# Kernel optimization log

Measured on AMD Instinct MI355X. Metric: run time of the kernel, lower is better.

Reference implementation:

```python
import jax, jax.numpy as jnp
import numpy as np

DIM = 192
HEADS = 6
WS = (4, 8, 8)  # window size (D, H, W)
N = WS[0] * WS[1] * WS[2]  # 256 tokens per window
NW = 64
B_ = 256  # batch * nW


def _relative_position_index(ws):
    d, h, w = ws
    coords = jnp.stack(jnp.meshgrid(jnp.arange(d), jnp.arange(h), jnp.arange(w), indexing='ij'))
    coords = coords.reshape(3, -1)  # (3, N)
    rel = coords[:, :, None] - coords[:, None, :]  # (3, N, N)
    rel = rel.transpose(1, 2, 0) + jnp.array([d - 1, h - 1, w - 1])
    idx = rel[..., 0] * ((2 * h - 1) * (2 * w - 1)) + rel[..., 1] * (2 * w - 1) + rel[..., 2]
    return idx.astype(jnp.int32)  # (N, N)


def setup_inputs() -> dict:
    key = jax.random.key(0)
    ks = jax.random.split(key, 7)
    table_rows = (2 * WS[0] - 1) * (2 * WS[1] - 1) * (2 * WS[2] - 1)  # 1575
    return {
        'x': jax.random.normal(ks[0], (B_, N, DIM), dtype=jnp.float32),
        'mask': jax.random.normal(ks[1], (NW, N, N), dtype=jnp.float32),
        'qkv_w': jax.random.normal(ks[2], (DIM, 3 * DIM), dtype=jnp.float32) * 0.02,
        'qkv_b': jnp.zeros((3 * DIM,), dtype=jnp.float32),
        'proj_w': jax.random.normal(ks[3], (DIM, DIM), dtype=jnp.float32) * 0.02,
        'proj_b': jnp.zeros((DIM,), dtype=jnp.float32),
        'bias_table': jax.random.normal(ks[4], (table_rows, HEADS), dtype=jnp.float32) * 0.02,
        'rel_index': _relative_position_index(WS),
    }


def reference(x, mask, qkv_w, qkv_b, proj_w, proj_b, bias_table, rel_index):
    B, Ntok, C = x.shape
    hd = C // HEADS
    scale = hd ** (-0.5)
    qkv = (x @ qkv_w + qkv_b).reshape(B, Ntok, 3, HEADS, hd)
    qkv = qkv.transpose(2, 0, 3, 1, 4)  # (3, B, H, N, hd)
    q, k, v = qkv[0], qkv[1], qkv[2]
    attn = jnp.einsum('bhnd,bhmd->bhnm', q * scale, k)  # (B, H, N, N)
    # gathered relative-position bias: (N, N, H) -> (H, N, N)
    bias = bias_table[rel_index.reshape(-1)].reshape(Ntok, Ntok, HEADS).transpose(2, 0, 1)
    attn = attn + bias[None]
    nW = mask.shape[0]
    attn = attn.reshape(B // nW, nW, HEADS, Ntok, Ntok) + mask[None, :, None]
    attn = attn.reshape(B, HEADS, Ntok, Ntok)
    attn = jax.nn.softmax(attn, axis=-1)
    out = jnp.einsum('bhnm,bhmd->bhnd', attn, v)  # (B, H, N, hd)
    out = out.transpose(0, 2, 1, 3).reshape(B, Ntok, C)
    out = out @ proj_w + proj_b
    return out
```

## Files before the change

### kernel.cpp

```cpp
#include <hip/hip_runtime.h>
#include <cstdint>
#include <math.h>

#define DIMC 192
#define NTOK 256
#define HEADS 6
#define HD 32
#define L2E 1.4426950408889634f

typedef __bf16 bf16x8 __attribute__((ext_vector_type(8)));
typedef __bf16 bf16x4 __attribute__((ext_vector_type(4)));
typedef float f32x4 __attribute__((ext_vector_type(4)));

__device__ __forceinline__ void gload_lds16(const __bf16* g, __bf16* l) {
    __builtin_amdgcn_global_load_lds((const __attribute__((address_space(1))) void*)g,
                                     (__attribute__((address_space(3))) void*)l, 16, 0, 0);
}

__global__ void prep(const float* __restrict__ x, __bf16* __restrict__ xb,
                     const float* __restrict__ qkv_w, __bf16* __restrict__ wqt,
                     const float* __restrict__ proj_w, __bf16* __restrict__ wpt,
                     const float* __restrict__ table, const int* __restrict__ rel,
                     __bf16* __restrict__ biasb) {
    const int bid = blockIdx.x, t = threadIdx.x;
    if (bid < 6144) {
        int i = bid * 256 + t;
        float4 a = ((const float4*)x)[i * 2];
        float4 b = ((const float4*)x)[i * 2 + 1];
        bf16x8 o = {(__bf16)a.x, (__bf16)a.y, (__bf16)a.z, (__bf16)a.w,
                    (__bf16)b.x, (__bf16)b.y, (__bf16)b.z, (__bf16)b.w};
        ((bf16x8*)xb)[i] = o;
    } else if (bid < 6576) {
        int i = (bid - 6144) * 256 + t;
        int n = i / DIMC, k = i - n * DIMC;
        wqt[i] = (__bf16)qkv_w[(size_t)k * 576 + n];
    } else if (bid < 6720) {
        int i = (bid - 6576) * 256 + t;
        int n = i / DIMC, k = i - n * DIMC;
        wpt[i] = (__bf16)proj_w[(size_t)k * DIMC + n];
    } else {
        int i = (bid - 6720) * 256 + t;
        int h = i >> 16;
        int r = i & 65535;
        biasb[i] = (__bf16)(table[rel[r] * 6 + h] * L2E);
    }
}

__launch_bounds__(256, 2)
__global__ void qkvbm(const __bf16* __restrict__ A, const __bf16* __restrict__ Wt,
                      const float* __restrict__ bias,
                      __bf16* __restrict__ qo, __bf16* __restrict__ ko, __bf16* __restrict__ vo,
                      const float* __restrict__ mask, const __bf16* __restrict__ biasb,
                      __bf16* __restrict__ bm) {
    __shared__ __bf16 As[256 * 64];
    __shared__ __bf16 Bs[96 * 64];
    const int t = threadIdx.x;
    const int lin = blockIdx.x;

    if (lin >= 1536) {
        int i = (lin - 1536) * 256 + t;
        int w = i >> 13, oct = i & 8191;
        float4 m0 = ((const float4*)mask)[(size_t)w * 16384 + oct * 2];
        float4 m1 = ((const float4*)mask)[(size_t)w * 16384 + oct * 2 + 1];
        #pragma unroll
        for (int h = 0; h < 6; ++h) {
            bf16x8 bb = ((const bf16x8*)biasb)[h * 8192 + oct];
            bf16x8 o = {(__bf16)(m0.x * L2E + (float)bb[0]), (__bf16)(m0.y * L2E + (float)bb[1]),
                        (__bf16)(m0.z * L2E + (float)bb[2]), (__bf16)(m0.w * L2E + (float)bb[3]),
                        (__bf16)(m1.x * L2E + (float)bb[4]), (__bf16)(m1.y * L2E + (float)bb[5]),
                        (__bf16)(m1.z * L2E + (float)bb[6]), (__bf16)(m1.w * L2E + (float)bb[7])};
            ((bf16x8*)bm)[(size_t)(w * 6 + h) * 8192 + oct] = o;
        }
        return;
    }

    const int wv = t >> 6, lane = t & 63;
    const int l16 = lane & 15, quad = lane >> 4;
    const int xcd = lin & 7, pos = lin >> 3;
    const int bx = pos % 6;
    const int by = xcd + (pos / 6) * 8;
    const int m0 = by * 256;
    const int j0 = bx * 96;

    f32x4 acc[4][6];
    #pragma unroll
    for (int mt = 0; mt < 4; ++mt)
        #pragma unroll
        for (int nt = 0; nt < 6; ++nt)
            acc[mt][nt] = (f32x4){0.f, 0.f, 0.f, 0.f};

    for (int kit = 0; kit < 3; ++kit) {
        const int k0 = kit * 64;
        #pragma unroll
        for (int gi = 0; gi < 8; ++gi) {
            int g = wv * 8 + gi;
            int cid = g * 64 + lane;
            int row = cid >> 3, kcs = cid & 7;
            int kcg = kcs ^ (row & 7);
            gload_lds16(A + (size_t)(m0 + row) * DIMC + k0 + kcg * 8, As + g * 512);
        }
        #pragma unroll
        for (int gi = 0; gi < 3; ++gi) {
            int g = wv * 3 + gi;
            int cid = g * 64 + lane;
            int n = cid >> 3, kcs = cid & 7;
            int kcg = kcs ^ (n & 7);
            gload_lds16(Wt + (size_t)(j0 + n) * DIMC + k0 + kcg * 8, Bs + g * 512);
        }
        __syncthreads();
        #pragma unroll
        for (int kk = 0; kk < 2; ++kk) {
            bf16x8 af[4], bfr[6];
            #pragma unroll
            for (int mt = 0; mt < 4; ++mt) {
                int row = wv * 64 + mt * 16 + l16;
                int ch = (kk * 4 + quad) ^ (row & 7);
                af[mt] = *(const bf16x8*)(As + row * 64 + ch * 8);
            }
            #pragma unroll
            for (int nt = 0; nt < 6; ++nt) {
                int n = nt * 16 + l16;
                int ch = (kk * 4 + quad) ^ (n & 7);
                bfr[nt] = *(const bf16x8*)(Bs + n * 64 + ch * 8);
            }
            #pragma unroll
            for (int mt = 0; mt < 4; ++mt)
                #pragma unroll
                for (int nt = 0; nt < 6; ++nt)
                    acc[mt][nt] = __builtin_amdgcn_mfma_f32_16x16x32_bf16(af[mt], bfr[nt], acc[mt][nt], 0, 0, 0);
        }
        __syncthreads();
    }

    const int which = bx >> 1;
    __bf16* outp = which == 0 ? qo : (which == 1 ? ko : vo);
    const float sc = which == 0 ? (0.17677669529663687f * L2E) : 1.0f;
    float bq[6];
    #pragma unroll
    for (int nt = 0; nt < 6; ++nt) bq[nt] = bias[j0 + nt * 16 + l16];
    const int cloc = (bx & 1) * 96;
    const int b = m0 >> 8;

    if (which != 2) {
        __bf16* tile = As + wv * 4096;
        const int TP = 104;
        #pragma unroll
        for (int mt = 0; mt < 4; ++mt) {
            #pragma unroll
            for (int nt = 0; nt < 6; ++nt)
                #pragma unroll
                for (int r = 0; r < 4; ++r)
                    tile[(quad * 4 + r) * TP + nt * 16 + l16] = (__bf16)((acc[mt][nt][r] + bq[nt]) * sc);
            int row = lane >> 2;
            #pragma unroll
            for (int it = 0; it < 3; ++it) {
                int c8 = (lane & 3) + it * 4;
                bf16x8 val = *(const bf16x8*)(tile + row * TP + c8 * 8);
                int n = wv * 64 + mt * 16 + row;
                int cw = cloc + c8 * 8;
                int h = cw >> 5, d0 = cw & 31;
                *(bf16x8*)(outp + (((size_t)b * HEADS + h) * NTOK + n) * HD + d0) = val;
            }
        }
    } else {
        __bf16* tileT = As + wv * 4096;
        #pragma unroll
        for (int mt = 0; mt < 4; ++mt) {
            #pragma unroll
            for (int nt = 0; nt < 6; ++nt)
                #pragma unroll
                for (int r = 0; r < 4; ++r)
                    tileT[(nt * 16 + l16) * 16 + quad * 4 + r] = (__bf16)(acc[mt][nt][r] + bq[nt]);
            int n0 = wv * 64 + mt * 16;
            #pragma unroll
            for (int it = 0; it < 3; ++it) {
                int qid = lane + 64 * it;
                int col = qid >> 1, half = qid & 1;
                bf16x8 val = *(const bf16x8*)(tileT + col * 16 + half * 8);
                int cw = cloc + col;
                int h = cw >> 5, d = cw & 31;
                *(bf16x8*)(outp + (((size_t)b * HEADS + h) * HD + d) * NTOK + n0 + half * 8) = val;
            }
        }
    }
}

__launch_bounds__(512, 6)
__global__ void attn_mfma(const __bf16* __restrict__ qg, const __bf16* __restrict__ kg,
                          const __bf16* __restrict__ vtg, const __bf16* __restrict__ bm,
                          __bf16* __restrict__ aout) {
    __shared__ __bf16 Ks[NTOK * 32];
    __shared__ __bf16 VTs[HD * 256];

    const int lin = blockIdx.x;
    const int xcd = lin & 7, pos = lin >> 3;
    const int g = xcd + (pos >> 2) * 8;
    const int i4 = pos & 3;
    const int h = g % 6, w = g / 6;
    const int b = i4 * 64 + w;
    const int bh = b * HEADS + h;

    const int t = threadIdx.x;
    const int wv = t >> 6, lane = t & 63;
    const int l16 = lane & 15, quad = lane >> 4;
    const int q0 = wv * 32;
    const size_t base = (size_t)bh * (NTOK * HD);

    #pragma unroll
    for (int it = 0; it < 2; ++it) {
        int grp = it * 8 + wv;
        int cid = grp * 64 + lane;
        int row = cid >> 2, cc = cid & 3;
        int scc = cc ^ (((row >> 1) & 1) | (((row >> 3) & 1) << 1));
        gload_lds16(kg + base + row * HD + scc * 8, Ks + grp * 512);
    }
    #pragma unroll
    for (int it = 0; it < 2; ++it) {
        int grp = it * 8 + wv;
        int cid = grp * 64 + lane;
        int row = cid >> 5, cc = cid & 31;
        int scc = cc ^ (row & 7);
        gload_lds16(vtg + base + row * NTOK + scc * 8, VTs + grp * 512);
    }
    __syncthreads();

    bf16x8 qf[2];
    #pragma unroll
    for (int qt = 0; qt < 2; ++qt)
        qf[qt] = *(const bf16x8*)(qg + base + (size_t)(q0 + qt * 16 + l16) * HD + quad * 8);

    f32x4 o[2][2];
    #pragma unroll
    for (int qt = 0; qt < 2; ++qt)
        #pragma unroll
        for (int dt = 0; dt < 2; ++dt)
            o[qt][dt] = (f32x4){0.f, 0.f, 0.f, 0.f};
    float rsum[2] = {};

    const __bf16* bmq = bm + (size_t)(w * 6 + h) * 65536 + (size_t)(q0 + l16) * 256 + quad * 8;
    const int kapb = 8 * (l16 >> 2) + (l16 & 3);
    const int ck = quad ^ ((l16 >> 1) & 1) ^ (((l16 >> 2) & 1) << 1);
    const int xv = l16 & 7;

    for (int c = 0; c < 8; ++c) {
        const int kb = c * 32;
        bf16x8 bmv[2];
        #pragma unroll
        for (int qt = 0; qt < 2; ++qt)
            bmv[qt] = *(const bf16x8*)(bmq + qt * 4096 + kb);
        bf16x8 kf[2];
        #pragma unroll
        for (int kt = 0; kt < 2; ++kt)
            kf[kt] = *(const bf16x8*)(Ks + (kb + kapb + 4 * kt) * 32 + ck * 8);
        bf16x8 vf[2];
        #pragma unroll
        for (int dt = 0; dt < 2; ++dt) {
            int cv = (c * 4 + quad) ^ xv;
            vf[dt] = *(const bf16x8*)(VTs + (dt * 16 + l16) * 256 + cv * 8);
        }

        #pragma unroll
        for (int qt = 0; qt < 2; ++qt) {
            bf16x8 pf;
            #pragma unroll
            for (int kt = 0; kt < 2; ++kt) {
                f32x4 ci;
                #pragma unroll
                for (int r = 0; r < 4; ++r)
                    ci[r] = (float)bmv[qt][kt * 4 + r];
                f32x4 s = __builtin_amdgcn_mfma_f32_16x16x32_bf16(kf[kt], qf[qt], ci, 0, 0, 0);
                #pragma unroll
                for (int r = 0; r < 4; ++r) {
                    float p = __builtin_amdgcn_exp2f(s[r]);
                    rsum[qt] += p;
                    pf[kt * 4 + r] = (__bf16)p;
                }
            }
            #pragma unroll
            for (int dt = 0; dt < 2; ++dt)
                o[qt][dt] = __builtin_amdgcn_mfma_f32_16x16x32_bf16(pf, vf[dt], o[qt][dt], 0, 0, 0);
        }
    }

    float rstot[2];
    #pragma unroll
    for (int qt = 0; qt < 2; ++qt) {
        float s = rsum[qt];
        s += __shfl_xor(s, 16);
        s += __shfl_xor(s, 32);
        rstot[qt] = 1.0f / s;
    }
    #pragma unroll
    for (int qt = 0; qt < 2; ++qt) {
        #pragma unroll
        for (int r = 0; r < 4; ++r) {
            float inv = __shfl(rstot[qt], (lane & 48) | (quad * 4 + r));
            int qrow = q0 + qt * 16 + quad * 4 + r;
            #pragma unroll
            for (int dt = 0; dt < 2; ++dt)
                aout[((size_t)b * NTOK + qrow) * DIMC + h * HD + dt * 16 + l16] =
                    (__bf16)(o[qt][dt][r] * inv);
        }
    }
}

__launch_bounds__(256, 2)
__global__ void proj_mfma(const __bf16* __restrict__ A, const __bf16* __restrict__ Wt,
                          const float* __restrict__ bias, float* __restrict__ out) {
    __shared__ __bf16 As[256 * 64];
    __shared__ __bf16 Bs[96 * 64];
    const int t = threadIdx.x;
    const int wv = t >> 6, lane = t & 63;
    const int l16 = lane & 15, quad = lane >> 4;

    const int lin = blockIdx.x + blockIdx.y * 2;
    const int xcd = lin & 7, pos = lin >> 3;
    const int bx = pos & 1;
    const int by = xcd + (pos >> 1) * 8;

    const int m0 = by * 256;
    const int j0 = bx * 96;

    f32x4 acc[4][6];
    #pragma unroll
    for (int mt = 0; mt < 4; ++mt)
        #pragma unroll
        for (int nt = 0; nt < 6; ++nt)
            acc[mt][nt] = (f32x4){0.f, 0.f, 0.f, 0.f};

    for (int kit = 0; kit < 3; ++kit) {
        const int k0 = kit * 64;
        #pragma unroll
        for (int gi = 0; gi < 8; ++gi) {
            int g = wv * 8 + gi;
            int cid = g * 64 + lane;
            int row = cid >> 3, kcs = cid & 7;
            int kcg = kcs ^ (row & 7);
            gload_lds16(A + (size_t)(m0 + row) * DIMC + k0 + kcg * 8, As + g * 512);
        }
        #pragma unroll
        for (int gi = 0; gi < 3; ++gi) {
            int g = wv * 3 + gi;
            int cid = g * 64 + lane;
            int n = cid >> 3, kcs = cid & 7;
            int kcg = kcs ^ (n & 7);
            gload_lds16(Wt + (size_t)(j0 + n) * DIMC + k0 + kcg * 8, Bs + g * 512);
        }
        __syncthreads();
        #pragma unroll
        for (int kk = 0; kk < 2; ++kk) {
            bf16x8 af[4], bfr[6];
            #pragma unroll
            for (int mt = 0; mt < 4; ++mt) {
                int row = wv * 64 + mt * 16 + l16;
                int ch = (kk * 4 + quad) ^ (row & 7);
                af[mt] = *(const bf16x8*)(As + row * 64 + ch * 8);
            }
            #pragma unroll
            for (int nt = 0; nt < 6; ++nt) {
                int n = nt * 16 + l16;
                int ch = (kk * 4 + quad) ^ (n & 7);
                bfr[nt] = *(const bf16x8*)(Bs + n * 64 + ch * 8);
            }
            #pragma unroll
            for (int mt = 0; mt < 4; ++mt)
                #pragma unroll
                for (int nt = 0; nt < 6; ++nt)
                    acc[mt][nt] = __builtin_amdgcn_mfma_f32_16x16x32_bf16(af[mt], bfr[nt], acc[mt][nt], 0, 0, 0);
        }
        __syncthreads();
    }

    #pragma unroll
    for (int nt = 0; nt < 6; ++nt) {
        int colg = j0 + nt * 16 + l16;
        float bv = bias[colg];
        #pragma unroll
        for (int mt = 0; mt < 4; ++mt)
            #pragma unroll
            for (int r = 0; r < 4; ++r) {
                int token = m0 + wv * 64 + mt * 16 + quad * 4 + r;
                out[(size_t)token * DIMC + colg] = acc[mt][nt][r] + bv;
            }
    }
}

extern "C" void kernel_launch(void* const* d_in, const int* in_sizes, int n_in,
                              void* d_out, int out_size, void* d_ws, size_t ws_size,
                              hipStream_t stream) {
    const float* x          = (const float*)d_in[0];
    const float* mask       = (const float*)d_in[1];
    const float* qkv_w      = (const float*)d_in[2];
    const float* qkv_b      = (const float*)d_in[3];
    const float* proj_w     = (const float*)d_in[4];
    const float* proj_b     = (const float*)d_in[5];
    const float* bias_table = (const float*)d_in[6];
    const int*   rel_index  = (const int*)d_in[7];

    char* ws = (char*)d_ws;
    __bf16* xb    = (__bf16*)(ws);
    __bf16* q     = (__bf16*)(ws + 25165824);
    __bf16* k     = (__bf16*)(ws + 50331648);
    __bf16* vT    = (__bf16*)(ws + 75497472);
    __bf16* biasb = (__bf16*)(ws + 100663296);
    __bf16* wqt   = (__bf16*)(ws + 102236160);
    __bf16* wpt   = (__bf16*)(ws + 102457344);
    __bf16* aoutb = xb;
    __bf16* bm    = (__bf16*)d_out;

    prep<<<8256, 256, 0, stream>>>(x, xb, qkv_w, wqt, proj_w, wpt, bias_table, rel_index, biasb);
    qkvbm<<<3584, 256, 0, stream>>>(xb, wqt, qkv_b, q, k, vT, mask, biasb, bm);
    attn_mfma<<<1536, 512, 0, stream>>>(q, k, vT, bm, aoutb);
    proj_mfma<<<dim3(2, 256), 256, 0, stream>>>(aoutb, wpt, proj_b, (float*)d_out);
}
```

Before: 206.5 us.

## Split precombined bias+mask tensor into separate bf16 mask and bias inputs

Stops materializing the full per-window-per-head bias+mask bf16 tensor in the QKV kernel. The prep kernel now converts the mask to scaled bf16 once per window, and the attention kernel loads mask and bias tiles separately and adds them in registers. This removes a large write and read-back of the expanded tensor. In exchange the inner loop issues twice as many global loads and does extra adds.

```diff
diff --git a/kernel.cpp b/kernel.cpp
--- a/kernel.cpp
+++ b/kernel.cpp
@@ -21,7 +21,8 @@
                      const float* __restrict__ qkv_w, __bf16* __restrict__ wqt,
                      const float* __restrict__ proj_w, __bf16* __restrict__ wpt,
                      const float* __restrict__ table, const int* __restrict__ rel,
-                     __bf16* __restrict__ biasb) {
+                     __bf16* __restrict__ biasb,
+                     const float* __restrict__ mask, __bf16* __restrict__ maskb) {
     const int bid = blockIdx.x, t = threadIdx.x;
     if (bid < 6144) {
         int i = bid * 256 + t;
@@ -38,41 +39,29 @@
         int i = (bid - 6576) * 256 + t;
         int n = i / DIMC, k = i - n * DIMC;
         wpt[i] = (__bf16)proj_w[(size_t)k * DIMC + n];
-    } else {
+    } else if (bid < 8256) {
         int i = (bid - 6720) * 256 + t;
         int h = i >> 16;
         int r = i & 65535;
         biasb[i] = (__bf16)(table[rel[r] * 6 + h] * L2E);
+    } else {
+        int i = (bid - 8256) * 256 + t;
+        float4 a = ((const float4*)mask)[(size_t)i * 2];
+        float4 b = ((const float4*)mask)[(size_t)i * 2 + 1];
+        bf16x8 o = {(__bf16)(a.x * L2E), (__bf16)(a.y * L2E), (__bf16)(a.z * L2E), (__bf16)(a.w * L2E),
+                    (__bf16)(b.x * L2E), (__bf16)(b.y * L2E), (__bf16)(b.z * L2E), (__bf16)(b.w * L2E)};
+        ((bf16x8*)maskb)[i] = o;
     }
 }
 
 __launch_bounds__(256, 2)
 __global__ void qkvbm(const __bf16* __restrict__ A, const __bf16* __restrict__ Wt,
                       const float* __restrict__ bias,
-                      __bf16* __restrict__ qo, __bf16* __restrict__ ko, __bf16* __restrict__ vo,
-                      const float* __restrict__ mask, const __bf16* __restrict__ biasb,
-                      __bf16* __restrict__ bm) {
+                      __bf16* __restrict__ qo, __bf16* __restrict__ ko, __bf16* __restrict__ vo) {
     __shared__ __bf16 As[256 * 64];
     __shared__ __bf16 Bs[96 * 64];
     const int t = threadIdx.x;
     const int lin = blockIdx.x;
-
-    if (lin >= 1536) {
-        int i = (lin - 1536) * 256 + t;
-        int w = i >> 13, oct = i & 8191;
-        float4 m0 = ((const float4*)mask)[(size_t)w * 16384 + oct * 2];
-        float4 m1 = ((const float4*)mask)[(size_t)w * 16384 + oct * 2 + 1];
-        #pragma unroll
-        for (int h = 0; h < 6; ++h) {
-            bf16x8 bb = ((const bf16x8*)biasb)[h * 8192 + oct];
-            bf16x8 o = {(__bf16)(m0.x * L2E + (float)bb[0]), (__bf16)(m0.y * L2E + (float)bb[1]),
-                        (__bf16)(m0.z * L2E + (float)bb[2]), (__bf16)(m0.w * L2E + (float)bb[3]),
-                        (__bf16)(m1.x * L2E + (float)bb[4]), (__bf16)(m1.y * L2E + (float)bb[5]),
-                        (__bf16)(m1.z * L2E + (float)bb[6]), (__bf16)(m1.w * L2E + (float)bb[7])};
-            ((bf16x8*)bm)[(size_t)(w * 6 + h) * 8192 + oct] = o;
-        }
-        return;
-    }
 
     const int wv = t >> 6, lane = t & 63;
     const int l16 = lane & 15, quad = lane >> 4;
@@ -187,8 +176,8 @@
 
 __launch_bounds__(512, 6)
 __global__ void attn_mfma(const __bf16* __restrict__ qg, const __bf16* __restrict__ kg,
-                          const __bf16* __restrict__ vtg, const __bf16* __restrict__ bm,
-                          __bf16* __restrict__ aout) {
+                          const __bf16* __restrict__ vtg, const __bf16* __restrict__ maskb,
+                          const __bf16* __restrict__ biasb, __bf16* __restrict__ aout) {
     __shared__ __bf16 Ks[NTOK * 32];
     __shared__ __bf16 VTs[HD * 256];
 
@@ -237,17 +226,20 @@
             o[qt][dt] = (f32x4){0.f, 0.f, 0.f, 0.f};
     float rsum[2] = {};
 
-    const __bf16* bmq = bm + (size_t)(w * 6 + h) * 65536 + (size_t)(q0 + l16) * 256 + quad * 8;
+    const __bf16* mq = maskb + (size_t)w * 65536 + (size_t)(q0 + l16) * 256 + quad * 8;
+    const __bf16* bq = biasb + (size_t)h * 65536 + (size_t)(q0 + l16) * 256 + quad * 8;
     const int kapb = 8 * (l16 >> 2) + (l16 & 3);
     const int ck = quad ^ ((l16 >> 1) & 1) ^ (((l16 >> 2) & 1) << 1);
     const int xv = l16 & 7;
 
     for (int c = 0; c < 8; ++c) {
         const int kb = c * 32;
-        bf16x8 bmv[2];
-        #pragma unroll
-        for (int qt = 0; qt < 2; ++qt)
-            bmv[qt] = *(const bf16x8*)(bmq + qt * 4096 + kb);
+        bf16x8 mv[2], bv[2];
+        #pragma unroll
+        for (int qt = 0; qt < 2; ++qt) {
+            mv[qt] = *(const bf16x8*)(mq + qt * 4096 + kb);
+            bv[qt] = *(const bf16x8*)(bq + qt * 4096 + kb);
+        }
         bf16x8 kf[2];
         #pragma unroll
         for (int kt = 0; kt < 2; ++kt)
@@ -267,7 +259,7 @@
                 f32x4 ci;
                 #pragma unroll
                 for (int r = 0; r < 4; ++r)
-                    ci[r] = (float)bmv[qt][kt * 4 + r];
+                    ci[r] = (float)mv[qt][kt * 4 + r] + (float)bv[qt][kt * 4 + r];
                 f32x4 s = __builtin_amdgcn_mfma_f32_16x16x32_bf16(kf[kt], qf[qt], ci, 0, 0, 0);
                 #pragma unroll
                 for (int r = 0; r < 4; ++r) {
@@ -403,13 +395,14 @@
     __bf16* k     = (__bf16*)(ws + 50331648);
     __bf16* vT    = (__bf16*)(ws + 75497472);
     __bf16* biasb = (__bf16*)(ws + 100663296);
-    __bf16* wqt   = (__bf16*)(ws + 102236160);
-    __bf16* wpt   = (__bf16*)(ws + 102457344);
+    __bf16* maskb = (__bf16*)(ws + 101449728);
+    __bf16* wqt   = (__bf16*)(ws + 109838336);
+    __bf16* wpt   = (__bf16*)(ws + 110059520);
     __bf16* aoutb = xb;
-    __bf16* bm    = (__bf16*)d_out;
-
-    prep<<<8256, 256, 0, stream>>>(x, xb, qkv_w, wqt, proj_w, wpt, bias_table, rel_index, biasb);
-    qkvbm<<<3584, 256, 0, stream>>>(xb, wqt, qkv_b, q, k, vT, mask, biasb, bm);
-    attn_mfma<<<1536, 512, 0, stream>>>(q, k, vT, bm, aoutb);
+
+    prep<<<10304, 256, 0, stream>>>(x, xb, qkv_w, wqt, proj_w, wpt,
+                                    bias_table, rel_index, biasb, mask, maskb);
+    qkvbm<<<1536, 256, 0, stream>>>(xb, wqt, qkv_b, q, k, vT);
+    attn_mfma<<<1536, 512, 0, stream>>>(q, k, vT, maskb, biasb, aoutb);
     proj_mfma<<<dim3(2, 256), 256, 0, stream>>>(aoutb, wpt, proj_b, (float*)d_out);
 }
```

After: 223.0 us. 1.08x slower.

## Move mask+bias precompute into prep kernel and split pure QKV GEMM kernel

Applied to the files above, without the earlier changes.

The combined mask-plus-relative-bias tensor is now built in the prep kernel, gathering bias_table directly through rel_index, so the intermediate biasb buffer and its round trip through memory go away. The QKV GEMM kernel no longer carries the extra mask blocks and runs only its GEMM tiles, with launch bounds raised to allow three blocks per CU. The trade-off is a scattered gather from the bias table in prep. The mask work now also shares a kernel with the conversion blocks instead of overlapping with GEMM blocks.

```diff
diff --git a/kernel.cpp b/kernel.cpp
--- a/kernel.cpp
+++ b/kernel.cpp
@@ -21,7 +21,7 @@
                      const float* __restrict__ qkv_w, __bf16* __restrict__ wqt,
                      const float* __restrict__ proj_w, __bf16* __restrict__ wpt,
                      const float* __restrict__ table, const int* __restrict__ rel,
-                     __bf16* __restrict__ biasb) {
+                     const float* __restrict__ mask, __bf16* __restrict__ bm) {
     const int bid = blockIdx.x, t = threadIdx.x;
     if (bid < 6144) {
         int i = bid * 256 + t;
@@ -40,39 +40,32 @@
         wpt[i] = (__bf16)proj_w[(size_t)k * DIMC + n];
     } else {
         int i = (bid - 6720) * 256 + t;
-        int h = i >> 16;
-        int r = i & 65535;
-        biasb[i] = (__bf16)(table[rel[r] * 6 + h] * L2E);
-    }
-}
-
-__launch_bounds__(256, 2)
-__global__ void qkvbm(const __bf16* __restrict__ A, const __bf16* __restrict__ Wt,
-                      const float* __restrict__ bias,
-                      __bf16* __restrict__ qo, __bf16* __restrict__ ko, __bf16* __restrict__ vo,
-                      const float* __restrict__ mask, const __bf16* __restrict__ biasb,
-                      __bf16* __restrict__ bm) {
+        int w = i >> 13, oct = i & 8191;
+        float4 m0 = ((const float4*)mask)[(size_t)w * 16384 + oct * 2];
+        float4 m1 = ((const float4*)mask)[(size_t)w * 16384 + oct * 2 + 1];
+        int4 r0 = ((const int4*)rel)[oct * 2];
+        int4 r1 = ((const int4*)rel)[oct * 2 + 1];
+        float mm[8] = {m0.x, m0.y, m0.z, m0.w, m1.x, m1.y, m1.z, m1.w};
+        int   rr[8] = {r0.x, r0.y, r0.z, r0.w, r1.x, r1.y, r1.z, r1.w};
+        #pragma unroll
+        for (int h = 0; h < 6; ++h) {
+            bf16x8 o;
+            #pragma unroll
+            for (int j = 0; j < 8; ++j)
+                o[j] = (__bf16)((mm[j] + table[rr[j] * 6 + h]) * L2E);
+            ((bf16x8*)bm)[(size_t)(w * 6 + h) * 8192 + oct] = o;
+        }
+    }
+}
+
+__launch_bounds__(256, 3)
+__global__ void qkv_mfma(const __bf16* __restrict__ A, const __bf16* __restrict__ Wt,
+                         const float* __restrict__ bias,
+                         __bf16* __restrict__ qo, __bf16* __restrict__ ko, __bf16* __restrict__ vo) {
     __shared__ __bf16 As[256 * 64];
     __shared__ __bf16 Bs[96 * 64];
     const int t = threadIdx.x;
     const int lin = blockIdx.x;
-
-    if (lin >= 1536) {
-        int i = (lin - 1536) * 256 + t;
-        int w = i >> 13, oct = i & 8191;
-        float4 m0 = ((const float4*)mask)[(size_t)w * 16384 + oct * 2];
-        float4 m1 = ((const float4*)mask)[(size_t)w * 16384 + oct * 2 + 1];
-        #pragma unroll
-        for (int h = 0; h < 6; ++h) {
-            bf16x8 bb = ((const bf16x8*)biasb)[h * 8192 + oct];
-            bf16x8 o = {(__bf16)(m0.x * L2E + (float)bb[0]), (__bf16)(m0.y * L2E + (float)bb[1]),
-                        (__bf16)(m0.z * L2E + (float)bb[2]), (__bf16)(m0.w * L2E + (float)bb[3]),
-                        (__bf16)(m1.x * L2E + (float)bb[4]), (__bf16)(m1.y * L2E + (float)bb[5]),
-                        (__bf16)(m1.z * L2E + (float)bb[6]), (__bf16)(m1.w * L2E + (float)bb[7])};
-            ((bf16x8*)bm)[(size_t)(w * 6 + h) * 8192 + oct] = o;
-        }
-        return;
-    }
 
     const int wv = t >> 6, lane = t & 63;
     const int l16 = lane & 15, quad = lane >> 4;
@@ -402,14 +395,13 @@
     __bf16* q     = (__bf16*)(ws + 25165824);
     __bf16* k     = (__bf16*)(ws + 50331648);
     __bf16* vT    = (__bf16*)(ws + 75497472);
-    __bf16* biasb = (__bf16*)(ws + 100663296);
-    __bf16* wqt   = (__bf16*)(ws + 102236160);
-    __bf16* wpt   = (__bf16*)(ws + 102457344);
+    __bf16* wqt   = (__bf16*)(ws + 100663296);
+    __bf16* wpt   = (__bf16*)(ws + 100884480);
     __bf16* aoutb = xb;
     __bf16* bm    = (__bf16*)d_out;
 
-    prep<<<8256, 256, 0, stream>>>(x, xb, qkv_w, wqt, proj_w, wpt, bias_table, rel_index, biasb);
-    qkvbm<<<3584, 256, 0, stream>>>(xb, wqt, qkv_b, q, k, vT, mask, biasb, bm);
+    prep<<<8768, 256, 0, stream>>>(x, xb, qkv_w, wqt, proj_w, wpt, bias_table, rel_index, mask, bm);
+    qkv_mfma<<<1536, 256, 0, stream>>>(xb, wqt, qkv_b, q, k, vT);
     attn_mfma<<<1536, 512, 0, stream>>>(q, k, vT, bm, aoutb);
     proj_mfma<<<dim3(2, 256), 256, 0, stream>>>(aoutb, wpt, proj_b, (float*)d_out);
 }
```

Result: slower. 211.0 us (+2.2%).
